# Performance work log

Measured on AMD Instinct MI355X. Metric: run time of the kernel, lower is better.

## Reference

```python
import jax, jax.numpy as jnp
import numpy as np

N_BOND = 100000      # number of 'bond' nodes in the batched graph
IN_DIM = 32
SPACE_NUM = 6
D = SPACE_NUM * IN_DIM  # 192; bo_merge='cat' keeps h at space_num*in_dim
N_ETYPES = 36        # len(prot_atom_ids) * len(drug_atom_ids) = 4 * 9
E_PER_TYPE = 30000   # edges per edge type
B = 256              # batch_size (number of graphs)


def setup_inputs() -> dict:
    key = jax.random.key(0)
    k1, k2, k3, k4, k5 = jax.random.split(key, 5)
    h = jax.random.normal(k1, (N_BOND, D), dtype=jnp.float32)
    # output_layer: nn.Linear(D, 1, bias=False)
    W_out = jax.random.normal(k2, (D, 1), dtype=jnp.float32) / np.sqrt(D)
    # per-edge-type source node ids (DGL copy_u gather indices)
    edge_src = jax.random.randint(k3, (N_ETYPES, E_PER_TYPE), 0, N_BOND, dtype=jnp.int32)
    # per-edge graph id; sorted within each type (mimics arange(B).repeat(batch_num_edges))
    edge_seg = jnp.sort(jax.random.randint(k4, (N_ETYPES, E_PER_TYPE), 0, B, dtype=jnp.int32), axis=1)
    mask_mat = jax.random.randint(k5, (B, N_ETYPES), 0, 2).astype(bool)
    return {"h": h, "W_out": W_out, "edge_src": edge_src,
            "edge_seg": edge_seg, "mask_mat": mask_mat}


def reference(h, W_out, edge_src, edge_seg, mask_mat):
    # Fused over all 36 edge types: global segment id = type * B + graph_id
    type_idx = jnp.arange(N_ETYPES, dtype=edge_seg.dtype)[:, None]        # [T,1]
    seg_global = (type_idx * B + edge_seg).reshape(-1)                    # [T*E]
    eh = h[edge_src.reshape(-1)]                                          # gather: [T*E, D]
    sums = jax.ops.segment_sum(eh, seg_global, num_segments=N_ETYPES * B)  # [T*B, D]
    graph_feat = sums.reshape(N_ETYPES, B, D).transpose(1, 0, 2)          # [B, T, D]
    graph_v = jnp.einsum('btd,do->bt', graph_feat, W_out)                 # [B, T]
    graph_v = jnp.where(mask_mat, jnp.float32(-1e9), graph_v)
    return jax.nn.softmax(graph_v, axis=1)
```

## Files before the change

kernel.cpp:

```cpp
#include <hip/hip_runtime.h>

#define N_BOND   100000
#define D_DIM    192
#define N_ETYPES 36
#define E_PER_TYPE 30000
#define BATCH    256
#define TOTAL_E  (N_ETYPES * E_PER_TYPE)
#define ACC_N    (N_ETYPES * BATCH)

__global__ void hv_kernel(const float* __restrict__ h, const float* __restrict__ W,
                          float* __restrict__ hv, float* __restrict__ acc) {
    int gid = blockIdx.x * blockDim.x + threadIdx.x;
    if (gid < ACC_N) acc[gid] = 0.f;

    int wave = gid >> 6;
    int lane = threadIdx.x & 63;
    int row  = wave * 4 + (lane >> 4);
    int ql   = lane & 15;
    if (row >= N_BOND) return;

    const float4* hp = (const float4*)(h + (size_t)row * D_DIM);
    const float4* wp = (const float4*)W;
    float v = 0.f;
#pragma unroll
    for (int k = 0; k < 3; ++k) {
        float4 a = hp[ql + 16 * k];
        float4 w = wp[ql + 16 * k];
        v += a.x * w.x + a.y * w.y + a.z * w.z + a.w * w.w;
    }
#pragma unroll
    for (int d = 8; d > 0; d >>= 1) v += __shfl_down(v, d, 64);
    if (ql == 0) hv[row] = v;
}

__global__ void edge_kernel(const int* __restrict__ edge_src,
                            const int* __restrict__ edge_seg,
                            const float* __restrict__ hv,
                            float* __restrict__ acc) {
    int tid  = blockIdx.x * blockDim.x + threadIdx.x;
    int lane = threadIdx.x & 63;
    int e0   = tid * 4;
    bool valid = (e0 < TOTAL_E);
    int ec = valid ? e0 : (TOTAL_E - 4);
    int t  = ec / E_PER_TYPE;

    int4 s4 = ((const int4*)edge_seg)[ec >> 2];
    int4 r4 = ((const int4*)edge_src)[ec >> 2];
    float v0 = valid ? hv[r4.x] : 0.f;
    float v1 = valid ? hv[r4.y] : 0.f;
    float v2 = valid ? hv[r4.z] : 0.f;
    float v3 = valid ? hv[r4.w] : 0.f;

    int base = t * BATCH;
    int k0 = base + s4.x, k1 = base + s4.y, k2 = base + s4.z, k3 = base + s4.w;

    int   ck = k0;
    float cv = v0;
    if (k1 == ck) cv += v1; else { atomicAdd(&acc[ck], cv); ck = k1; cv = v1; }
    if (k2 == ck) cv += v2; else { atomicAdd(&acc[ck], cv); ck = k2; cv = v2; }
    if (k3 == ck) cv += v3; else { atomicAdd(&acc[ck], cv); ck = k3; cv = v3; }

#pragma unroll
    for (int d = 1; d < 64; d <<= 1) {
        float uv = __shfl_up(cv, d, 64);
        int   uk = __shfl_up(ck, d, 64);
        if (lane >= d && uk == ck) cv += uv;
    }
    int nk = __shfl_down(ck, 1, 64);
    if (lane == 63 || nk != ck) atomicAdd(&acc[ck], cv);
}

__global__ void softmax_kernel(const float* __restrict__ acc,
                               const void* __restrict__ mask,
                               float* __restrict__ out) {
    int b = threadIdx.x;

    const unsigned int* mi = (const unsigned int*)mask;
    bool is_u8 = false;
#pragma unroll
    for (int i = 0; i < 16; ++i) is_u8 |= (mi[i] > 1u);
    const unsigned char* m8  = (const unsigned char*)mask;
    const int*           m32 = (const int*)mask;

    float v[N_ETYPES];
    float mx = -1e30f;
#pragma unroll
    for (int t = 0; t < N_ETYPES; ++t) {
        float x = acc[t * BATCH + b];
        bool masked = is_u8 ? (m8[b * N_ETYPES + t] != 0)
                            : (m32[b * N_ETYPES + t] != 0);
        x = masked ? -1e9f : x;
        v[t] = x;
        mx = fmaxf(mx, x);
    }
    float s = 0.f;
#pragma unroll
    for (int t = 0; t < N_ETYPES; ++t) { v[t] = expf(v[t] - mx); s += v[t]; }
    float inv = 1.f / s;
#pragma unroll
    for (int t = 0; t < N_ETYPES; ++t) out[b * N_ETYPES + t] = v[t] * inv;
}

extern "C" void kernel_launch(void* const* d_in, const int* in_sizes, int n_in,
                              void* d_out, int out_size, void* d_ws, size_t ws_size,
                              hipStream_t stream) {
    const float* h        = (const float*)d_in[0];
    const float* W        = (const float*)d_in[1];
    const int*   edge_src = (const int*)d_in[2];
    const int*   edge_seg = (const int*)d_in[3];
    const void*  mask     = d_in[4];
    float*       out      = (float*)d_out;

    float* hv  = (float*)d_ws;
    float* acc = (float*)((char*)d_ws + 400128);

    hipLaunchKernelGGL(hv_kernel, dim3(N_BOND / 16), dim3(256), 0, stream, h, W, hv, acc);

    int eb = (TOTAL_E / 4 + 255) / 256;
    hipLaunchKernelGGL(edge_kernel, dim3(eb), dim3(256), 0, stream, edge_src, edge_seg, hv, acc);

    hipLaunchKernelGGL(softmax_kernel, dim3(1), dim3(256), 0, stream, acc, mask, out);
}
```

Measured before the change: 130.9 us.

## Fuse softmax into edge kernel via last-block counter and process 8 edges per thread

Merges the single-block softmax kernel into the edge scatter kernel, using a global done counter so the last-finishing block runs the softmax, which removes one kernel launch. Each thread also handles 8 edges instead of 4, with a serial run-length merge before the wave scan, so fewer atomics are issued and the grid is halved. The counter is zeroed in hv_kernel by widening its zero-init by one element. The cost is a threadfence plus an atomic per block, and the softmax now waits on the tail of the edge grid.

```diff
diff --git a/kernel.cpp b/kernel.cpp
--- a/kernel.cpp
+++ b/kernel.cpp
@@ -7,11 +7,14 @@
 #define BATCH    256
 #define TOTAL_E  (N_ETYPES * E_PER_TYPE)
 #define ACC_N    (N_ETYPES * BATCH)
+#define EPT      8
+#define EDGE_THREADS (TOTAL_E / EPT)
+#define EDGE_BLOCKS  ((EDGE_THREADS + 255) / 256)
 
 __global__ void hv_kernel(const float* __restrict__ h, const float* __restrict__ W,
                           float* __restrict__ hv, float* __restrict__ acc) {
     int gid = blockIdx.x * blockDim.x + threadIdx.x;
-    if (gid < ACC_N) acc[gid] = 0.f;
+    if (gid <= ACC_N) acc[gid] = 0.f;
 
     int wave = gid >> 6;
     int lane = threadIdx.x & 63;
@@ -33,32 +36,46 @@
     if (ql == 0) hv[row] = v;
 }
 
-__global__ void edge_kernel(const int* __restrict__ edge_src,
-                            const int* __restrict__ edge_seg,
-                            const float* __restrict__ hv,
-                            float* __restrict__ acc) {
+__global__ void edge_softmax_kernel(const int* __restrict__ edge_src,
+                                    const int* __restrict__ edge_seg,
+                                    const float* __restrict__ hv,
+                                    float* __restrict__ acc,
+                                    int* __restrict__ done,
+                                    const void* __restrict__ mask,
+                                    float* __restrict__ out) {
     int tid  = blockIdx.x * blockDim.x + threadIdx.x;
     int lane = threadIdx.x & 63;
-    int e0   = tid * 4;
+    int e0   = tid * EPT;
     bool valid = (e0 < TOTAL_E);
-    int ec = valid ? e0 : (TOTAL_E - 4);
+    int ec = valid ? e0 : (TOTAL_E - EPT);
     int t  = ec / E_PER_TYPE;
 
-    int4 s4 = ((const int4*)edge_seg)[ec >> 2];
-    int4 r4 = ((const int4*)edge_src)[ec >> 2];
-    float v0 = valid ? hv[r4.x] : 0.f;
-    float v1 = valid ? hv[r4.y] : 0.f;
-    float v2 = valid ? hv[r4.z] : 0.f;
-    float v3 = valid ? hv[r4.w] : 0.f;
+    const int4* sp = (const int4*)(edge_seg + ec);
+    const int4* rp = (const int4*)(edge_src + ec);
+    int4 sa = sp[0], sb = sp[1];
+    int4 ra = rp[0], rb = rp[1];
+
+    float v[EPT];
+    v[0] = valid ? hv[ra.x] : 0.f;
+    v[1] = valid ? hv[ra.y] : 0.f;
+    v[2] = valid ? hv[ra.z] : 0.f;
+    v[3] = valid ? hv[ra.w] : 0.f;
+    v[4] = valid ? hv[rb.x] : 0.f;
+    v[5] = valid ? hv[rb.y] : 0.f;
+    v[6] = valid ? hv[rb.z] : 0.f;
+    v[7] = valid ? hv[rb.w] : 0.f;
 
     int base = t * BATCH;
-    int k0 = base + s4.x, k1 = base + s4.y, k2 = base + s4.z, k3 = base + s4.w;
+    int k[EPT] = { base + sa.x, base + sa.y, base + sa.z, base + sa.w,
+                   base + sb.x, base + sb.y, base + sb.z, base + sb.w };
 
-    int   ck = k0;
-    float cv = v0;
-    if (k1 == ck) cv += v1; else { atomicAdd(&acc[ck], cv); ck = k1; cv = v1; }
-    if (k2 == ck) cv += v2; else { atomicAdd(&acc[ck], cv); ck = k2; cv = v2; }
-    if (k3 == ck) cv += v3; else { atomicAdd(&acc[ck], cv); ck = k3; cv = v3; }
+    int   ck = k[0];
+    float cv = v[0];
+#pragma unroll
+    for (int i = 1; i < EPT; ++i) {
+        if (k[i] == ck) cv += v[i];
+        else { atomicAdd(&acc[ck], cv); ck = k[i]; cv = v[i]; }
+    }
 
 #pragma unroll
     for (int d = 1; d < 64; d <<= 1) {
@@ -68,11 +85,18 @@
     }
     int nk = __shfl_down(ck, 1, 64);
     if (lane == 63 || nk != ck) atomicAdd(&acc[ck], cv);
-}
 
-__global__ void softmax_kernel(const float* __restrict__ acc,
-                               const void* __restrict__ mask,
-                               float* __restrict__ out) {
+    __threadfence();
+    __syncthreads();
+    __shared__ int is_last;
+    if (threadIdx.x == 0) {
+        int prev = __hip_atomic_fetch_add(done, 1, __ATOMIC_ACQ_REL,
+                                          __HIP_MEMORY_SCOPE_AGENT);
+        is_last = (prev == (int)gridDim.x - 1);
+    }
+    __syncthreads();
+    if (!is_last) return;
+
     int b = threadIdx.x;
 
     const unsigned int* mi = (const unsigned int*)mask;
@@ -82,23 +106,24 @@
     const unsigned char* m8  = (const unsigned char*)mask;
     const int*           m32 = (const int*)mask;
 
-    float v[N_ETYPES];
+    float vv[N_ETYPES];
     float mx = -1e30f;
 #pragma unroll
-    for (int t = 0; t < N_ETYPES; ++t) {
-        float x = acc[t * BATCH + b];
-        bool masked = is_u8 ? (m8[b * N_ETYPES + t] != 0)
-                            : (m32[b * N_ETYPES + t] != 0);
+    for (int tt = 0; tt < N_ETYPES; ++tt) {
+        float x = __hip_atomic_load(&acc[tt * BATCH + b], __ATOMIC_RELAXED,
+                                    __HIP_MEMORY_SCOPE_AGENT);
+        bool masked = is_u8 ? (m8[b * N_ETYPES + tt] != 0)
+                            : (m32[b * N_ETYPES + tt] != 0);
         x = masked ? -1e9f : x;
-        v[t] = x;
+        vv[tt] = x;
         mx = fmaxf(mx, x);
     }
     float s = 0.f;
 #pragma unroll
-    for (int t = 0; t < N_ETYPES; ++t) { v[t] = expf(v[t] - mx); s += v[t]; }
+    for (int tt = 0; tt < N_ETYPES; ++tt) { vv[tt] = expf(vv[tt] - mx); s += vv[tt]; }
     float inv = 1.f / s;
 #pragma unroll
-    for (int t = 0; t < N_ETYPES; ++t) out[b * N_ETYPES + t] = v[t] * inv;
+    for (int tt = 0; tt < N_ETYPES; ++tt) out[b * N_ETYPES + tt] = vv[tt] * inv;
 }
 
 extern "C" void kernel_launch(void* const* d_in, const int* in_sizes, int n_in,
@@ -111,13 +136,12 @@
     const void*  mask     = d_in[4];
     float*       out      = (float*)d_out;
 
-    float* hv  = (float*)d_ws;
-    float* acc = (float*)((char*)d_ws + 400128);
+    float* hv   = (float*)d_ws;
+    float* acc  = (float*)((char*)d_ws + 400128);
+    int*   done = (int*)(acc + ACC_N);
 
     hipLaunchKernelGGL(hv_kernel, dim3(N_BOND / 16), dim3(256), 0, stream, h, W, hv, acc);
 
-    int eb = (TOTAL_E / 4 + 255) / 256;
-    hipLaunchKernelGGL(edge_kernel, dim3(eb), dim3(256), 0, stream, edge_src, edge_seg, hv, acc);
-
-    hipLaunchKernelGGL(softmax_kernel, dim3(1), dim3(256), 0, stream, acc, mask, out);
+    hipLaunchKernelGGL(edge_softmax_kernel, dim3(EDGE_BLOCKS), dim3(256), 0, stream,
+                       edge_src, edge_seg, hv, acc, done, mask, out);
 }
```

New measurement: 172.1 us. +31.5%, slower.
